# Performance work log

Measured on AMD Instinct MI355X. Metric: run time of the kernel, lower is better.

The kernel has to match this reference:

```python
import jax, jax.numpy as jnp
import numpy as np

NR, NC = 30, 20  # grid rows/cols
H = W = 512
B = 4
CIN = 55

def _conv(x, w, b, dil, pad):
    y = jax.lax.conv_general_dilated(
        x, w, window_strides=(1, 1), padding=[(pad, pad), (pad, pad)],
        rhs_dilation=(dil, dil), dimension_numbers=('NCHW', 'OIHW', 'NCHW'))
    return y + b[None, :, None, None]

def _cell_means(t, cell, n_cells):
    # t: [B,C,H,W]; torch.mean over the WHOLE slice (batch+channel+cell pixels)
    b, c = t.shape[0], t.shape[1]
    s = t.sum(axis=(0, 1))                              # [H,W]
    sums = jax.ops.segment_sum(s.ravel(), cell.ravel(), num_segments=n_cells)
    cnts = jax.ops.segment_sum(jnp.ones((t.shape[2] * t.shape[3],), t.dtype),
                               cell.ravel(), num_segments=n_cells) * (b * c)
    return sums / cnts                                   # [n_cells]

def setup_inputs() -> dict:
    key = jax.random.key(0)
    ks = jax.random.split(key, 16)
    x = jax.random.normal(ks[0], (B, CIN, H, W), jnp.float32)
    # segment ids per row/col, nondecreasing, every id present
    row_seg = jnp.sort(jnp.concatenate([jnp.arange(NR, dtype=jnp.int32),
                                        jax.random.randint(ks[1], (H - NR,), 0, NR, jnp.int32)]))
    col_seg = jnp.sort(jnp.concatenate([jnp.arange(NC, dtype=jnp.int32),
                                        jax.random.randint(ks[2], (W - NC,), 0, NC, jnp.int32)]))
    def wb(k, o, i, kh, kw):
        fan = i * kh * kw
        lim = 1.0 / np.sqrt(fan)
        k1, k2 = jax.random.split(k)
        w = jax.random.uniform(k1, (o, i, kh, kw), jnp.float32, -lim, lim)
        b = jax.random.uniform(k2, (o,), jnp.float32, -lim, lim)
        return w, b
    w1, b1 = wb(ks[3], 6, CIN, 5, 5)
    w2, b2 = wb(ks[4], 6, CIN, 5, 5)
    w3, b3 = wb(ks[5], 6, CIN, 5, 5)
    wt, bt = wb(ks[6], 36, 18, 1, 1)
    wbm, bbm = wb(ks[7], 1, 18, 1, 1)
    return {'x': x, 'row_seg': row_seg, 'col_seg': col_seg,
            'w1': w1, 'b1': b1, 'w2': w2, 'b2': b2, 'w3': w3, 'b3': b3,
            'wt': wt, 'bt': bt, 'wb': wbm, 'bb': bbm}

def reference(x, row_seg, col_seg, w1, b1, w2, b2, w3, b3, wt, bt, wb, bb):
    x1 = jax.nn.relu(_conv(x, w1, b1, 1, 2))
    x2 = jax.nn.relu(_conv(x, w2, b2, 2, 4))
    x3 = jax.nn.relu(_conv(x, w3, b3, 3, 6))
    feat = jnp.concatenate([x1, x2, x3], axis=1)          # [B,18,H,W]
    top = _conv(feat, wt, bt, 1, 0)                        # [B,36,H,W]
    bot = _conv(feat, wb, bb, 1, 0)                        # [B,1,H,W]
    cell = row_seg[:, None] * NC + col_seg[None, :]        # [H,W]
    n_cells = NR * NC
    top_m = _cell_means(top, cell, n_cells)                # [600]
    bot_m = _cell_means(bot, cell, n_cells)                # [600]
    b = x.shape[0]
    top_out = jnp.broadcast_to(top_m[cell][None, None], (b, top.shape[1], top.shape[2], top.shape[3]))
    bot_out = jnp.broadcast_to(bot_m[cell][None, None], (b, 1, bot.shape[2], bot.shape[3]))
    pools = jnp.broadcast_to(jax.nn.sigmoid(bot_m).reshape(1, 1, NR, NC), (b, 1, NR, NC))
    out_x = jnp.concatenate([top_out, feat, jax.nn.sigmoid(bot_out)], axis=1)  # [B,55,H,W]
    return out_x, pools
```

## Files before the change

kernel.cpp:

```cpp
#include <hip/hip_runtime.h>
#include <math.h>

#define HW 512
#define NPIX (HW*HW)
#define NB 4
#define NCIN 55
#define OUTX_SIZE (NB*55*NPIX)

#define WA_OFF 0
#define WSUM_OFF 37632
#define BTSUM_OFF 37650
#define S_OFF 37664
#define TM_OFF 38864
#define SBM_OFF 39464

#define BY 16
#define BX 32
#define LROWS 28
#define LSTRIDE 49
#define CELLS (LROWS*LSTRIDE)
#define NLD 22
#define LDSC 1408
#define NSTEP 7
#define NCB 7

#define PH 524
#define PW 528
#define CBBYTES (PH*PW*16)

#define PREP_WBLK 147
#define PPK_TOT (NB*7*PH*(PW/8))

typedef _Float16 half2v __attribute__((ext_vector_type(2)));
typedef __attribute__((ext_vector_type(8))) _Float16 f16x8;
typedef __attribute__((ext_vector_type(4))) float f32x4;

__device__ __forceinline__ uint pack_f16x2(float a, float b) {
  return __builtin_bit_cast(uint, __builtin_amdgcn_cvt_pkrtz(a, b));
}

__device__ __forceinline__ void gload16(const void* g, void* l) {
  __builtin_amdgcn_global_load_lds(
      (const __attribute__((address_space(1))) void*)g,
      (__attribute__((address_space(3))) void*)l, 16, 0, 0);
}

__global__ __launch_bounds__(256) void prep_prepack_kernel(
    const float* __restrict__ x,
    const float* __restrict__ w1, const float* __restrict__ w2, const float* __restrict__ w3,
    const float* __restrict__ wt, const float* __restrict__ bt,
    float* __restrict__ ws, float* __restrict__ out)
{
  const int blk = blockIdx.x;
  const int tid = threadIdx.x;
  if (blk < PREP_WBLK) {
    const int e = blk * 256 + tid;
    uint* wp = (uint*)(ws + WA_OFF);
    int u = e & 3;
    int rest = e >> 2;
    int lane = rest & 63;
    int idx = rest >> 6;
    int step = idx % 7;
    int cbg = idx / 7;
    int cb = cbg % 7;
    int g = cbg / 7;
    int oc = lane & 15;
    int kg = lane >> 4;
    int tap = step * 4 + kg;
    int c = cb * 8 + 2 * u;
    const float* wsrc = (g == 0) ? w1 : (g == 1) ? w2 : w3;
    float lo = 0.f, hi = 0.f;
    if (oc < 6 && tap < 25) {
      if (c < NCIN)     lo = wsrc[(oc * NCIN + c) * 25 + tap];
      if (c + 1 < NCIN) hi = wsrc[(oc * NCIN + c + 1) * 25 + tap];
    }
    wp[e] = pack_f16x2(lo, hi);
    if (e < 1200) ws[S_OFF + e] = 0.f;
    if (blk == 0) {
      if (tid < 18) {
        float s = 0.f;
        for (int o = 0; o < 36; o++) s += wt[o * 18 + tid];
        ws[WSUM_OFF + tid] = s;
      }
      if (tid == 18) {
        float s = 0.f;
        for (int o = 0; o < 36; o++) s += bt[o];
        ws[BTSUM_OFF] = s;
      }
    }
    return;
  }
  const uint idx = (uint)(blk - PREP_WBLK) * 256u + (uint)tid;
  if (idx >= (uint)PPK_TOT) return;
  const uint pw8 = idx % 66u;
  const uint r1 = idx / 66u;
  const uint py = r1 % 524u;
  const uint r2 = r1 / 524u;
  const uint cb = r2 % 7u;
  const uint b  = r2 / 7u;
  const int gy = (int)py - 6;
  const int gx = (int)(pw8 << 3) - 8;
  const bool in = ((unsigned)gy < (unsigned)HW) && (gx >= 0) && (gx < HW);
  const int c0 = cb * 8;
  char* dst = (char*)(out + ((size_t)(b * 55) << 18))
            + (size_t)cb * CBBYTES + ((size_t)py * PW + (pw8 << 3)) * 16;
  if (!in) {
    uint4 z; z.x = z.y = z.z = z.w = 0u;
#pragma unroll
    for (int p = 0; p < 8; p++) *(uint4*)(dst + p * 16) = z;
    return;
  }
  const float* bp = x + (((size_t)(b * NCIN + c0)) << 18) + (size_t)gy * HW + gx;
  float4 f[8][2];
#pragma unroll
  for (int q = 0; q < 8; q++) {
    f[q][0].x = f[q][0].y = f[q][0].z = f[q][0].w = 0.f;
    f[q][1].x = f[q][1].y = f[q][1].z = f[q][1].w = 0.f;
  }
  if (cb < 6u) {
#pragma unroll
    for (int q = 0; q < 8; q++) {
      f[q][0] = *(const float4*)(bp + ((size_t)q << 18));
      f[q][1] = *(const float4*)(bp + ((size_t)q << 18) + 4);
    }
  } else {
#pragma unroll
    for (int q = 0; q < 7; q++) {
      f[q][0] = *(const float4*)(bp + ((size_t)q << 18));
      f[q][1] = *(const float4*)(bp + ((size_t)q << 18) + 4);
    }
  }
#pragma unroll
  for (int h = 0; h < 2; h++) {
    const float* fp = (const float*)&f[0][0];
#pragma unroll
    for (int p = 0; p < 4; p++) {
      uint4 u;
      u.x = pack_f16x2(((const float*)&f[0][h])[p], ((const float*)&f[1][h])[p]);
      u.y = pack_f16x2(((const float*)&f[2][h])[p], ((const float*)&f[3][h])[p]);
      u.z = pack_f16x2(((const float*)&f[4][h])[p], ((const float*)&f[5][h])[p]);
      u.w = pack_f16x2(((const float*)&f[6][h])[p], ((const float*)&f[7][h])[p]);
      *(uint4*)(dst + (h * 4 + p) * 16) = u;
    }
    (void)fp;
  }
}

__global__ __launch_bounds__(256, 2) void conv_kernel(
    const uint* wA, const float* bias1, const float* bias2, const float* bias3,
    const int* __restrict__ row_seg, const int* __restrict__ col_seg,
    const float* __restrict__ wsum18, const float* __restrict__ wb18,
    float* __restrict__ S, float* out)
{
  __shared__ uint xs[2 * LDSC * 4];
  __shared__ float bins[1200];
  __shared__ float swb[54];
  const int tid = threadIdx.x;
  const int lane = tid & 63;
  const int wv = tid >> 6;
  const int h0 = blockIdx.y * BY, w0 = blockIdx.x * BX;
  const int bz = blockIdx.z;
  const int col = lane & 15;
  const int kg  = lane >> 4;

  const char* xb = (const char*)out + (((size_t)(bz * 55)) << 20);
  const uint4* wA4 = (const uint4*)wA;

  for (int e = tid; e < 1200; e += 256) bins[e] = 0.f;
  if (tid < 18) swb[tid] = wsum18[tid];
  else if (tid < 36) swb[tid] = wb18[tid - 18];
  else if (tid < 54) {
    int k = tid - 36;
    int g = k / 6, o = k - g * 6;
    const float* bp = (g == 0) ? bias1 : (g == 1) ? bias2 : bias3;
    swb[tid] = bp[o];
  }

  uint voff[6];
#pragma unroll
  for (int t = 0; t < 6; t++) {
    int ld = wv * 6 + t;
    int l = ld * 64 + lane;
    if (l > CELLS - 1) l = CELLS - 1;
    int row = l / LSTRIDE;
    int c = l - row * LSTRIDE;
    if (c > 47) c = 47;
    voff[t] = (uint)(((h0 + row) * PW) + (w0 + c)) * 16u;
  }

  int so[3][7];
#pragma unroll
  for (int g = 0; g < 3; g++) {
#pragma unroll
    for (int s = 0; s < 7; s++) {
      int tap = s * 4 + kg;
      int dr = 0, dc = 0;
      if (tap < 25) { int q5 = tap / 5; dr = q5 - 2; dc = tap - q5 * 5 - 2; }
      so[g][s] = ((dr * LSTRIDE + dc) * (g + 1)) << 2;
    }
  }

  f32x4 acc[3][8];
#pragma unroll
  for (int g = 0; g < 3; g++)
#pragma unroll
    for (int nt = 0; nt < 8; nt++) acc[g][nt] = (f32x4){0.f, 0.f, 0.f, 0.f};

#pragma unroll
  for (int t = 0; t < 6; t++) {
    int ld = wv * 6 + t;
    if (ld < NLD) gload16(xb + voff[t], (char*)xs + ld * 1024);
  }
  __syncthreads();

  int cur = 0;
#pragma unroll 1
  for (int cb = 0; cb < NCB; cb++) {
    if (cb < NCB - 1) {
      const char* sb = xb + (size_t)(cb + 1) * CBBYTES;
      char* db = (char*)(xs + (cur ^ 1) * (LDSC * 4));
#pragma unroll
      for (int t = 0; t < 6; t++) {
        int ld = wv * 6 + t;
        if (ld < NLD) gload16(sb + voff[t], db + ld * 1024);
      }
    }
    const uint* xsb = xs + cur * (LDSC * 4);
#pragma unroll
    for (int g = 0; g < 3; g++) {
      const uint4* wp4 = wA4 + (size_t)((g * NCB + cb) * NSTEP) * 64 + lane;
      f16x8 af[7];
#pragma unroll
      for (int s = 0; s < 7; s++)
        af[s] = __builtin_bit_cast(f16x8, wp4[(size_t)s * 64]);
#pragma unroll
      for (int nt = 0; nt < 8; nt++) {
        const int bd = (((6 + (wv << 2) + (nt >> 1)) * LSTRIDE)
                       + (8 + ((nt & 1) << 4) + col)) << 2;
        f32x4 a = acc[g][nt];
#pragma unroll
        for (int s = 0; s < 7; s++) {
          uint4 tv = *(const uint4*)&xsb[bd + so[g][s]];
          a = __builtin_amdgcn_mfma_f32_16x16x32_f16(
                af[s], __builtin_bit_cast(f16x8, tv), a, 0, 0, 0);
        }
        acc[g][nt] = a;
      }
    }
    __syncthreads();
    cur ^= 1;
  }

#pragma unroll
  for (int nt = 0; nt < 8; nt++) {
    const int y = h0 + (wv << 2) + (nt >> 1);
    const int xx = w0 + ((nt & 1) << 4) + col;
    const size_t pix = (size_t)y * HW + xx;
    float stv = 0.f, sbv = 0.f;
#pragma unroll
    for (int g = 0; g < 3; g++) {
#pragma unroll
      for (int r = 0; r < 4; r++) {
        int slot = (kg << 2) + r;
        if (slot < 6) {
          int k18 = g * 6 + slot;
          float v = fmaxf(acc[g][nt][r] + swb[36 + k18], 0.f);
          out[(((size_t)(bz * 55 + 36 + k18)) << 18) + pix] = v;
          stv = fmaf(swb[k18], v, stv);
          sbv = fmaf(swb[18 + k18], v, sbv);
        }
      }
    }
    stv += __shfl_xor(stv, 16);
    stv += __shfl_xor(stv, 32);
    sbv += __shfl_xor(sbv, 16);
    sbv += __shfl_xor(sbv, 32);
    if (lane < 16) {
      int cell = row_seg[y] * 20 + col_seg[xx];
      atomicAdd(&bins[cell * 2], stv);
      atomicAdd(&bins[cell * 2 + 1], sbv);
    }
  }
  __syncthreads();
  for (int e = tid; e < 1200; e += 256) {
    float v = bins[e];
    if (v != 0.f) atomicAdd(&S[e], v);
  }
}

__global__ __launch_bounds__(1024) void finalize_kernel(
    const int* __restrict__ row_seg, const int* __restrict__ col_seg,
    const float* __restrict__ S, const float* __restrict__ btsum,
    const float* __restrict__ bb, float* __restrict__ tm,
    float* __restrict__ sbm, float* __restrict__ out)
{
  __shared__ int rowcnt[30], colcnt[20];
  const int t = threadIdx.x;
  if (t < 30) rowcnt[t] = 0;
  if (t >= 32 && t < 52) colcnt[t - 32] = 0;
  __syncthreads();
  if (t < 512) atomicAdd(&rowcnt[row_seg[t]], 1);
  else atomicAdd(&colcnt[col_seg[t - 512]], 1);
  __syncthreads();
  if (t < 600) {
    int r = t / 20, c = t - r * 20;
    float cnt = (float)(rowcnt[r] * colcnt[c]);
    float topm = S[2 * t] / (cnt * 144.f) + btsum[0] * (1.f / 36.f);
    float botm = S[2 * t + 1] / (cnt * 4.f) + bb[0];
    tm[t] = topm;
    float s = 1.f / (1.f + expf(-botm));
    sbm[t] = s;
#pragma unroll
    for (int b = 0; b < 4; b++) out[OUTX_SIZE + b * 600 + t] = s;
  }
}

__global__ __launch_bounds__(256) void fill_kernel(
    const int* __restrict__ row_seg, const int* __restrict__ col_seg,
    const float* __restrict__ tm, const float* __restrict__ sbm,
    float* __restrict__ out)
{
  const int idx = blockIdx.x * 256 + threadIdx.x;
  const int b = idx >> 16;
  const int p4 = idx & 65535;
  const int h = p4 >> 7, w = (p4 & 127) << 2;
  const int rs = row_seg[h] * 20;
  float4 tmv, sbv;
  {
    int c0 = rs + col_seg[w + 0];
    int c1 = rs + col_seg[w + 1];
    int c2 = rs + col_seg[w + 2];
    int c3 = rs + col_seg[w + 3];
    tmv.x = tm[c0]; tmv.y = tm[c1]; tmv.z = tm[c2]; tmv.w = tm[c3];
    sbv.x = sbm[c0]; sbv.y = sbm[c1]; sbv.z = sbm[c2]; sbv.w = sbm[c3];
  }
  const size_t hw = (size_t)h * HW + w;
  float* base = out + (((size_t)(b * 55)) << 18) + hw;
#pragma unroll
  for (int ch = 0; ch < 36; ch++) *(float4*)(base + ((size_t)ch << 18)) = tmv;
  *(float4*)(base + ((size_t)54 << 18)) = sbv;
}

extern "C" void kernel_launch(void* const* d_in, const int* in_sizes, int n_in,
                              void* d_out, int out_size, void* d_ws, size_t ws_size,
                              hipStream_t stream) {
  const float* x       = (const float*)d_in[0];
  const int*   row_seg = (const int*)d_in[1];
  const int*   col_seg = (const int*)d_in[2];
  const float* w1 = (const float*)d_in[3];
  const float* b1 = (const float*)d_in[4];
  const float* w2 = (const float*)d_in[5];
  const float* b2 = (const float*)d_in[6];
  const float* w3 = (const float*)d_in[7];
  const float* b3 = (const float*)d_in[8];
  const float* wt = (const float*)d_in[9];
  const float* bt = (const float*)d_in[10];
  const float* wb = (const float*)d_in[11];
  const float* bb = (const float*)d_in[12];
  float* out = (float*)d_out;
  float* ws  = (float*)d_ws;

  const int ppk_blocks = PREP_WBLK + (PPK_TOT + 255) / 256;
  prep_prepack_kernel<<<ppk_blocks, 256, 0, stream>>>(x, w1, w2, w3, wt, bt,
                                                      ws, out);

  dim3 g1(HW / BX, HW / BY, NB);
  conv_kernel<<<g1, 256, 0, stream>>>((const uint*)(ws + WA_OFF),
                                      b1, b2, b3, row_seg, col_seg,
                                      ws + WSUM_OFF, wb, ws + S_OFF, out);

  finalize_kernel<<<1, 1024, 0, stream>>>(row_seg, col_seg, ws + S_OFF,
                                          ws + BTSUM_OFF, bb,
                                          ws + TM_OFF, ws + SBM_OFF, out);

  fill_kernel<<<NB * NPIX / 1024, 256, 0, stream>>>(row_seg, col_seg,
                                                    ws + TM_OFF, ws + SBM_OFF, out);
}
```

Before: 655.3 us.

## Fuse fp32-to-fp16 input packing into conv kernel, dropping the prepack pass

```diff
diff --git a/kernel.cpp b/kernel.cpp
--- a/kernel.cpp
+++ b/kernel.cpp
@@ -19,17 +19,10 @@
 #define LROWS 28
 #define LSTRIDE 49
 #define CELLS (LROWS*LSTRIDE)
-#define NLD 22
-#define LDSC 1408
-#define NSTEP 7
+#define NSLOT 336
 #define NCB 7
 
-#define PH 524
-#define PW 528
-#define CBBYTES (PH*PW*16)
-
 #define PREP_WBLK 147
-#define PPK_TOT (NB*7*PH*(PW/8))
 
 typedef _Float16 half2v __attribute__((ext_vector_type(2)));
 typedef __attribute__((ext_vector_type(8))) _Float16 f16x8;
@@ -39,120 +32,57 @@
   return __builtin_bit_cast(uint, __builtin_amdgcn_cvt_pkrtz(a, b));
 }
 
-__device__ __forceinline__ void gload16(const void* g, void* l) {
-  __builtin_amdgcn_global_load_lds(
-      (const __attribute__((address_space(1))) void*)g,
-      (__attribute__((address_space(3))) void*)l, 16, 0, 0);
-}
-
-__global__ __launch_bounds__(256) void prep_prepack_kernel(
-    const float* __restrict__ x,
+__global__ __launch_bounds__(256) void prep_kernel(
     const float* __restrict__ w1, const float* __restrict__ w2, const float* __restrict__ w3,
     const float* __restrict__ wt, const float* __restrict__ bt,
-    float* __restrict__ ws, float* __restrict__ out)
+    float* __restrict__ ws)
 {
   const int blk = blockIdx.x;
   const int tid = threadIdx.x;
-  if (blk < PREP_WBLK) {
-    const int e = blk * 256 + tid;
-    uint* wp = (uint*)(ws + WA_OFF);
-    int u = e & 3;
-    int rest = e >> 2;
-    int lane = rest & 63;
-    int idx = rest >> 6;
-    int step = idx % 7;
-    int cbg = idx / 7;
-    int cb = cbg % 7;
-    int g = cbg / 7;
-    int oc = lane & 15;
-    int kg = lane >> 4;
-    int tap = step * 4 + kg;
-    int c = cb * 8 + 2 * u;
-    const float* wsrc = (g == 0) ? w1 : (g == 1) ? w2 : w3;
-    float lo = 0.f, hi = 0.f;
-    if (oc < 6 && tap < 25) {
-      if (c < NCIN)     lo = wsrc[(oc * NCIN + c) * 25 + tap];
-      if (c + 1 < NCIN) hi = wsrc[(oc * NCIN + c + 1) * 25 + tap];
-    }
-    wp[e] = pack_f16x2(lo, hi);
-    if (e < 1200) ws[S_OFF + e] = 0.f;
-    if (blk == 0) {
-      if (tid < 18) {
-        float s = 0.f;
-        for (int o = 0; o < 36; o++) s += wt[o * 18 + tid];
-        ws[WSUM_OFF + tid] = s;
-      }
-      if (tid == 18) {
-        float s = 0.f;
-        for (int o = 0; o < 36; o++) s += bt[o];
-        ws[BTSUM_OFF] = s;
-      }
-    }
-    return;
-  }
-  const uint idx = (uint)(blk - PREP_WBLK) * 256u + (uint)tid;
-  if (idx >= (uint)PPK_TOT) return;
-  const uint pw8 = idx % 66u;
-  const uint r1 = idx / 66u;
-  const uint py = r1 % 524u;
-  const uint r2 = r1 / 524u;
-  const uint cb = r2 % 7u;
-  const uint b  = r2 / 7u;
-  const int gy = (int)py - 6;
-  const int gx = (int)(pw8 << 3) - 8;
-  const bool in = ((unsigned)gy < (unsigned)HW) && (gx >= 0) && (gx < HW);
-  const int c0 = cb * 8;
-  char* dst = (char*)(out + ((size_t)(b * 55) << 18))
-            + (size_t)cb * CBBYTES + ((size_t)py * PW + (pw8 << 3)) * 16;
-  if (!in) {
-    uint4 z; z.x = z.y = z.z = z.w = 0u;
-#pragma unroll
-    for (int p = 0; p < 8; p++) *(uint4*)(dst + p * 16) = z;
-    return;
-  }
-  const float* bp = x + (((size_t)(b * NCIN + c0)) << 18) + (size_t)gy * HW + gx;
-  float4 f[8][2];
-#pragma unroll
-  for (int q = 0; q < 8; q++) {
-    f[q][0].x = f[q][0].y = f[q][0].z = f[q][0].w = 0.f;
-    f[q][1].x = f[q][1].y = f[q][1].z = f[q][1].w = 0.f;
-  }
-  if (cb < 6u) {
-#pragma unroll
-    for (int q = 0; q < 8; q++) {
-      f[q][0] = *(const float4*)(bp + ((size_t)q << 18));
-      f[q][1] = *(const float4*)(bp + ((size_t)q << 18) + 4);
-    }
-  } else {
-#pragma unroll
-    for (int q = 0; q < 7; q++) {
-      f[q][0] = *(const float4*)(bp + ((size_t)q << 18));
-      f[q][1] = *(const float4*)(bp + ((size_t)q << 18) + 4);
-    }
-  }
-#pragma unroll
-  for (int h = 0; h < 2; h++) {
-    const float* fp = (const float*)&f[0][0];
-#pragma unroll
-    for (int p = 0; p < 4; p++) {
-      uint4 u;
-      u.x = pack_f16x2(((const float*)&f[0][h])[p], ((const float*)&f[1][h])[p]);
-      u.y = pack_f16x2(((const float*)&f[2][h])[p], ((const float*)&f[3][h])[p]);
-      u.z = pack_f16x2(((const float*)&f[4][h])[p], ((const float*)&f[5][h])[p]);
-      u.w = pack_f16x2(((const float*)&f[6][h])[p], ((const float*)&f[7][h])[p]);
-      *(uint4*)(dst + (h * 4 + p) * 16) = u;
-    }
-    (void)fp;
+  const int e = blk * 256 + tid;
+  uint* wp = (uint*)(ws + WA_OFF);
+  int u = e & 3;
+  int rest = e >> 2;
+  int lane = rest & 63;
+  int idx = rest >> 6;
+  int step = idx % 7;
+  int cbg = idx / 7;
+  int cb = cbg % 7;
+  int g = cbg / 7;
+  int oc = lane & 15;
+  int kg = lane >> 4;
+  int tap = step * 4 + kg;
+  int c = cb * 8 + 2 * u;
+  const float* wsrc = (g == 0) ? w1 : (g == 1) ? w2 : w3;
+  float lo = 0.f, hi = 0.f;
+  if (oc < 6 && tap < 25) {
+    if (c < NCIN)     lo = wsrc[(oc * NCIN + c) * 25 + tap];
+    if (c + 1 < NCIN) hi = wsrc[(oc * NCIN + c + 1) * 25 + tap];
+  }
+  wp[e] = pack_f16x2(lo, hi);
+  if (e < 1200) ws[S_OFF + e] = 0.f;
+  if (blk == 0) {
+    if (tid < 18) {
+      float s = 0.f;
+      for (int o = 0; o < 36; o++) s += wt[o * 18 + tid];
+      ws[WSUM_OFF + tid] = s;
+    }
+    if (tid == 18) {
+      float s = 0.f;
+      for (int o = 0; o < 36; o++) s += bt[o];
+      ws[BTSUM_OFF] = s;
+    }
   }
 }
 
 __global__ __launch_bounds__(256, 2) void conv_kernel(
-    const uint* wA, const float* bias1, const float* bias2, const float* bias3,
+    const float* __restrict__ x, const uint* wA,
+    const float* bias1, const float* bias2, const float* bias3,
     const int* __restrict__ row_seg, const int* __restrict__ col_seg,
     const float* __restrict__ wsum18, const float* __restrict__ wb18,
     float* __restrict__ S, float* out)
 {
-  __shared__ uint xs[2 * LDSC * 4];
+  __shared__ uint xs[2 * CELLS * 4];
   __shared__ float bins[1200];
   __shared__ float swb[54];
   const int tid = threadIdx.x;
@@ -163,7 +93,7 @@
   const int col = lane & 15;
   const int kg  = lane >> 4;
 
-  const char* xb = (const char*)out + (((size_t)(bz * 55)) << 20);
+  const float* xbase = x + ((size_t)(bz * NCIN) << 18);
   const uint4* wA4 = (const uint4*)wA;
 
   for (int e = tid; e < 1200; e += 256) bins[e] = 0.f;
@@ -176,28 +106,13 @@
     swb[tid] = bp[o];
   }
 
-  uint voff[6];
-#pragma unroll
-  for (int t = 0; t < 6; t++) {
-    int ld = wv * 6 + t;
-    int l = ld * 64 + lane;
-    if (l > CELLS - 1) l = CELLS - 1;
-    int row = l / LSTRIDE;
-    int c = l - row * LSTRIDE;
-    if (c > 47) c = 47;
-    voff[t] = (uint)(((h0 + row) * PW) + (w0 + c)) * 16u;
-  }
-
-  int so[3][7];
-#pragma unroll
-  for (int g = 0; g < 3; g++) {
-#pragma unroll
-    for (int s = 0; s < 7; s++) {
-      int tap = s * 4 + kg;
-      int dr = 0, dc = 0;
-      if (tap < 25) { int q5 = tap / 5; dr = q5 - 2; dc = tap - q5 * 5 - 2; }
-      so[g][s] = ((dr * LSTRIDE + dc) * (g + 1)) << 2;
-    }
+  int bofs[7];
+#pragma unroll
+  for (int s = 0; s < 7; s++) {
+    int tap = s * 4 + kg;
+    int dr = 0, dc = 0;
+    if (tap < 25) { int q5 = tap / 5; dr = q5 - 2; dc = tap - q5 * 5 - 2; }
+    bofs[s] = (dr * LSTRIDE + dc) << 2;
   }
 
   f32x4 acc[3][8];
@@ -206,33 +121,67 @@
 #pragma unroll
     for (int nt = 0; nt < 8; nt++) acc[g][nt] = (f32x4){0.f, 0.f, 0.f, 0.f};
 
-#pragma unroll
-  for (int t = 0; t < 6; t++) {
-    int ld = wv * 6 + t;
-    if (ld < NLD) gload16(xb + voff[t], (char*)xs + ld * 1024);
+  for (int e = tid; e < NSLOT; e += 256) {
+    int srow = e / 12, scg = e - srow * 12;
+    int sgy = h0 - 6 + srow, sgx = w0 - 8 + (scg << 2);
+    bool sin = ((unsigned)sgy < (unsigned)HW) && ((unsigned)sgx < (unsigned)HW);
+    float4 sr[8];
+#pragma unroll
+    for (int q = 0; q < 8; q++) { sr[q].x = sr[q].y = sr[q].z = sr[q].w = 0.f; }
+    if (sin) {
+      const float* sp = xbase + (size_t)sgy * HW + sgx;
+#pragma unroll
+      for (int q = 0; q < 8; q++) sr[q] = *(const float4*)(sp + ((size_t)q << 18));
+    }
+    int cd = (srow * LSTRIDE + (scg << 2)) << 2;
+#pragma unroll
+    for (int p = 0; p < 4; p++) {
+      uint4 u;
+      u.x = pack_f16x2(((const float*)&sr[0])[p], ((const float*)&sr[1])[p]);
+      u.y = pack_f16x2(((const float*)&sr[2])[p], ((const float*)&sr[3])[p]);
+      u.z = pack_f16x2(((const float*)&sr[4])[p], ((const float*)&sr[5])[p]);
+      u.w = pack_f16x2(((const float*)&sr[6])[p], ((const float*)&sr[7])[p]);
+      *(uint4*)&xs[cd + 4 * p] = u;
+    }
   }
   __syncthreads();
 
   int cur = 0;
 #pragma unroll 1
   for (int cb = 0; cb < NCB; cb++) {
-    if (cb < NCB - 1) {
-      const char* sb = xb + (size_t)(cb + 1) * CBBYTES;
-      char* db = (char*)(xs + (cur ^ 1) * (LDSC * 4));
-#pragma unroll
-      for (int t = 0; t < 6; t++) {
-        int ld = wv * 6 + t;
-        if (ld < NLD) gload16(sb + voff[t], db + ld * 1024);
+    const uint* xsb = xs + cur * (CELLS * 4);
+    const bool pf = (cb < NCB - 1) && (tid < 112);
+    const int c0n = (cb + 1) * 8;
+#pragma unroll
+    for (int g = 0; g < 3; g++) {
+      float4 sr[8];
+      int srow = 0, scg = 0;
+#pragma unroll
+      for (int q = 0; q < 8; q++) { sr[q].x = sr[q].y = sr[q].z = sr[q].w = 0.f; }
+      if (pf) {
+        int slot = g * 112 + tid;
+        srow = slot / 12; scg = slot - srow * 12;
+        int sgy = h0 - 6 + srow, sgx = w0 - 8 + (scg << 2);
+        if (((unsigned)sgy < (unsigned)HW) && ((unsigned)sgx < (unsigned)HW)) {
+          const float* sp = xbase + ((size_t)c0n << 18) + (size_t)sgy * HW + sgx;
+          if (cb < NCB - 2) {
+#pragma unroll
+            for (int q = 0; q < 8; q++)
+              sr[q] = *(const float4*)(sp + ((size_t)q << 18));
+          } else {
+#pragma unroll
+            for (int q = 0; q < 7; q++)
+              sr[q] = *(const float4*)(sp + ((size_t)q << 18));
+          }
+        }
       }
-    }
-    const uint* xsb = xs + cur * (LDSC * 4);
-#pragma unroll
-    for (int g = 0; g < 3; g++) {
-      const uint4* wp4 = wA4 + (size_t)((g * NCB + cb) * NSTEP) * 64 + lane;
+
+      const uint4* wp4 = wA4 + (size_t)((g * NCB + cb) * 7) * 64 + lane;
       f16x8 af[7];
 #pragma unroll
       for (int s = 0; s < 7; s++)
         af[s] = __builtin_bit_cast(f16x8, wp4[(size_t)s * 64]);
+
 #pragma unroll
       for (int nt = 0; nt < 8; nt++) {
         const int bd = (((6 + (wv << 2) + (nt >> 1)) * LSTRIDE)
@@ -240,11 +189,25 @@
         f32x4 a = acc[g][nt];
 #pragma unroll
         for (int s = 0; s < 7; s++) {
-          uint4 tv = *(const uint4*)&xsb[bd + so[g][s]];
+          uint4 tv = *(const uint4*)&xsb[bd + bofs[s] * (g + 1)];
           a = __builtin_amdgcn_mfma_f32_16x16x32_f16(
                 af[s], __builtin_bit_cast(f16x8, tv), a, 0, 0, 0);
         }
         acc[g][nt] = a;
+      }
+
+      if (pf) {
+        uint* db = xs + (cur ^ 1) * (CELLS * 4);
+        int cd = (srow * LSTRIDE + (scg << 2)) << 2;
+#pragma unroll
+        for (int p = 0; p < 4; p++) {
+          uint4 u;
+          u.x = pack_f16x2(((const float*)&sr[0])[p], ((const float*)&sr[1])[p]);
+          u.y = pack_f16x2(((const float*)&sr[2])[p], ((const float*)&sr[3])[p]);
+          u.z = pack_f16x2(((const float*)&sr[4])[p], ((const float*)&sr[5])[p]);
+          u.w = pack_f16x2(((const float*)&sr[6])[p], ((const float*)&sr[7])[p]);
+          *(uint4*)&db[cd + 4 * p] = u;
+        }
       }
     }
     __syncthreads();
@@ -360,12 +323,10 @@
   float* out = (float*)d_out;
   float* ws  = (float*)d_ws;
 
-  const int ppk_blocks = PREP_WBLK + (PPK_TOT + 255) / 256;
-  prep_prepack_kernel<<<ppk_blocks, 256, 0, stream>>>(x, w1, w2, w3, wt, bt,
-                                                      ws, out);
+  prep_kernel<<<PREP_WBLK, 256, 0, stream>>>(w1, w2, w3, wt, bt, ws);
 
   dim3 g1(HW / BX, HW / BY, NB);
-  conv_kernel<<<g1, 256, 0, stream>>>((const uint*)(ws + WA_OFF),
+  conv_kernel<<<g1, 256, 0, stream>>>(x, (const uint*)(ws + WA_OFF),
                                       b1, b2, b3, row_seg, col_seg,
                                       ws + WSUM_OFF, wb, ws + S_OFF, out);
 
```

New measurement: 613.8 us. 6.3% less time.
